# Kernel tuning notes

Hardware: AMD Instinct MI355X
Metric: run time of the kernel (lower is better)

## Reference

```python
import jax, jax.numpy as jnp
import numpy as np

N = 2097152
N_LAYERS = 32
N_SUB = 8


def setup_inputs() -> dict:
    key = jax.random.key(0)
    k1, k2, k3, k4 = jax.random.split(key, 4)
    return {
        "x": jax.random.normal(k1, (N, 2), dtype=jnp.float32),
        "act_w": 0.05 * jax.random.normal(k2, (N_LAYERS,), dtype=jnp.float32),
        "bias_b": 0.05 * jax.random.normal(k3, (N_LAYERS, 2), dtype=jnp.float32),
        "lin_w": 0.05 * jax.random.normal(k4, (N_LAYERS, N_SUB), dtype=jnp.float32),
    }


def _forward_chain(q, p, act_w, bias_b, lin_w):
    # Apply Modules[0..end] with inverse=0.
    n_layers, n_sub = lin_w.shape
    for i in range(n_layers):
        # activation module: up adds w*tanh(p) to q, low adds w*tanh(q) to p
        if i % 2 == 0:
            q = q + act_w[i] * jnp.tanh(p)
        else:
            p = p + act_w[i] * jnp.tanh(q)
        # bias module (inserted at j == 0)
        q = q + bias_b[i, 0]
        p = p + bias_b[i, 1]
        # linear shear modules
        for j in range(n_sub):
            if j % 2 == 0:   # linear_module_up: q += w*p
                q = q + lin_w[i, j] * p
            else:            # linear_module_low: p += w*q
                p = p + lin_w[i, j] * q
    return q, p


def _inverse_chain(q, p, act_w, bias_b, lin_w):
    # Apply all modules in reverse order with inverse=1 (negated weights).
    n_layers, n_sub = lin_w.shape
    for i in reversed(range(n_layers)):
        for j in reversed(range(n_sub)):
            if j % 2 == 0:
                q = q - lin_w[i, j] * p
            else:
                p = p - lin_w[i, j] * q
        q = q - bias_b[i, 0]
        p = p - bias_b[i, 1]
        if i % 2 == 0:
            q = q - act_w[i] * jnp.tanh(p)
        else:
            p = p - act_w[i] * jnp.tanh(q)
    return q, p


def reference(x, act_w, bias_b, lin_w):
    q, p = x[..., 0], x[..., 1]
    q, p = _forward_chain(q, p, act_w, bias_b, lin_w)
    # time reversal: multiply by [1, -1]
    p = -p
    q, p = _inverse_chain(q, p, act_w, bias_b, lin_w)
    # final module-0 inverse is included in _inverse_chain; scale by [1, -1]
    return jnp.stack([q, -p], axis=-1)
```

## Files before the change

kernel.cpp:

```cpp
#include <hip/hip_runtime.h>

constexpr int NL = 32;
constexpr int PPT = 4;

typedef float v2f __attribute__((ext_vector_type(2)));

__device__ __forceinline__ v2f splat(float a) { v2f r; r.x = a; r.y = a; return r; }
__device__ __forceinline__ v2f fma2(v2f a, v2f b, v2f c) { return __builtin_elementwise_fma(a, b, c); }
__device__ __forceinline__ v2f sfma(float s, v2f b, v2f c) { return __builtin_elementwise_fma(splat(s), b, c); }

__device__ __forceinline__ v2f tanh_poly2(v2f x) {
    v2f t = __builtin_elementwise_min(__builtin_elementwise_max(x, splat(-3.4f)), splat(3.4f));
    v2f s = t * t;
    v2f u = fma2(s, splat(2.3524e-06f), splat(-1.000059e-04f));
    u = fma2(s, u, splat(1.7302740e-03f));
    u = fma2(s, u, splat(-1.5874717e-02f));
    u = fma2(s, u, splat(8.5976700e-02f));
    u = fma2(s, u, splat(-3.0595090e-01f));
    u = fma2(s, u, splat(9.9691910e-01f));
    return t * u;
}

__global__ void build_tables(const float* __restrict__ act_w,
                             const float* __restrict__ bias_b,
                             const float* __restrict__ lin_w,
                             float* __restrict__ tab)
{
    int t = threadIdx.x;
    if (t >= NL) return;
    float m00 = 1.f, m01 = 0.f, m10 = 0.f, m11 = 1.f;
    #pragma unroll
    for (int j = 0; j < 8; ++j) {
        float w = lin_w[t * 8 + j];
        if ((j & 1) == 0) { m00 = fmaf(w, m10, m00); m01 = fmaf(w, m11, m01); }
        else              { m10 = fmaf(w, m00, m10); m11 = fmaf(w, m01, m11); }
    }
    float b0 = bias_b[2 * t], b1 = bias_b[2 * t + 1];
    float aw = act_w[t];
    float* f = &tab[t * 16];
    f[0] = m00; f[1] = m01; f[2] = m10; f[3] = m11;
    f[4] = fmaf(m00, b0, m01 * b1);
    f[5] = fmaf(m10, b0, m11 * b1);
    f[6] = aw; f[7] = 0.f;
    f[8]  = m11; f[9]  = -m01; f[10] = -m10; f[11] = m00;
    f[12] = -b0; f[13] = -b1; f[14] = -aw; f[15] = 0.f;
}

__global__ __launch_bounds__(256) void sympnet_main(
    const float* __restrict__ x,
    const float* __restrict__ tab,
    float* __restrict__ out)
{
    int gid = blockIdx.x * blockDim.x + threadIdx.x;
    const float4* x4 = (const float4*)x;
    float4* out4 = (float4*)out;
    long base = (long)gid * (PPT / 2);

    v2f Q[PPT / 2], P[PPT / 2];
    #pragma unroll
    for (int k = 0; k < PPT / 2; ++k) {
        float4 v = x4[base + k];
        Q[k].x = v.x; P[k].x = v.y;
        Q[k].y = v.z; P[k].y = v.w;
    }

    #pragma unroll 1
    for (int i = 0; i < NL; i += 2) {
        const float* f = &tab[i * 16];
        float m00=f[0], m01=f[1], m10=f[2], m11=f[3], C0=f[4], C1=f[5], T=f[6];
        const float* g = &tab[(i + 1) * 16];
        float n00=g[0], n01=g[1], n10=g[2], n11=g[3], E0=g[4], E1=g[5], U=g[6];
        #pragma unroll
        for (int k = 0; k < PPT / 2; ++k) {
            v2f Qa = sfma(T, tanh_poly2(P[k]), Q[k]);
            v2f Qn = sfma(m00, Qa, sfma(m01, P[k], splat(C0)));
            v2f Pn = sfma(m10, Qa, sfma(m11, P[k], splat(C1)));
            v2f Pa = sfma(U, tanh_poly2(Qn), Pn);
            Q[k] = sfma(n00, Qn, sfma(n01, Pa, splat(E0)));
            P[k] = sfma(n10, Qn, sfma(n11, Pa, splat(E1)));
        }
    }

    #pragma unroll
    for (int k = 0; k < PPT / 2; ++k) P[k] = -P[k];

    #pragma unroll 1
    for (int i = NL - 1; i > 0; i -= 2) {
        const float* g = &tab[i * 16 + 8];
        float n00=g[0], n01=g[1], n10=g[2], n11=g[3], E0=g[4], E1=g[5], U=g[6];
        const float* f = &tab[(i - 1) * 16 + 8];
        float m00=f[0], m01=f[1], m10=f[2], m11=f[3], C0=f[4], C1=f[5], T=f[6];
        #pragma unroll
        for (int k = 0; k < PPT / 2; ++k) {
            v2f Qn = sfma(n00, Q[k], sfma(n01, P[k], splat(E0)));
            v2f Pn = sfma(n10, Q[k], sfma(n11, P[k], splat(E1)));
            Pn = sfma(U, tanh_poly2(Qn), Pn);
            v2f Q2 = sfma(m00, Qn, sfma(m01, Pn, splat(C0)));
            v2f P2 = sfma(m10, Qn, sfma(m11, Pn, splat(C1)));
            Q[k] = sfma(T, tanh_poly2(P2), Q2);
            P[k] = P2;
        }
    }

    #pragma unroll
    for (int k = 0; k < PPT / 2; ++k) {
        float4 o;
        o.x = Q[k].x; o.y = -P[k].x;
        o.z = Q[k].y; o.w = -P[k].y;
        out4[base + k] = o;
    }
}

extern "C" void kernel_launch(void* const* d_in, const int* in_sizes, int n_in,
                              void* d_out, int out_size, void* d_ws, size_t ws_size,
                              hipStream_t stream) {
    const float* x      = (const float*)d_in[0];
    const float* act_w  = (const float*)d_in[1];
    const float* bias_b = (const float*)d_in[2];
    const float* lin_w  = (const float*)d_in[3];
    float* out = (float*)d_out;
    float* tab = (float*)d_ws;

    build_tables<<<1, 64, 0, stream>>>(act_w, bias_b, lin_w, tab);

    int npts = in_sizes[0] / 2;
    int nthreads = npts / PPT;
    int blocks = (nthreads + 255) / 256;
    sympnet_main<<<blocks, 256, 0, stream>>>(x, tab, out);
}
```

Baseline: 105.4 us.

## Use inline-asm packed FMAs with SGPR-pair operands and eight points per thread

Forces v_pk_fma_f32 through inline asm, with table weights stored as duplicated float pairs so they can be read as SGPR-pair operands. This avoids splat moves into VGPRs. It also folds the time-reversal sign flip into the inverse table, uses fmed3 for the clamp, and doubles the points per thread to 8 with launch bounds set for occupancy. The risks are higher register pressure and inline asm that blocks compiler scheduling. The launch now drops the rounding up of the block count, so it assumes N divides evenly.

```diff
diff --git a/kernel.cpp b/kernel.cpp
--- a/kernel.cpp
+++ b/kernel.cpp
@@ -1,33 +1,46 @@
 #include <hip/hip_runtime.h>
-
-constexpr int NL = 32;
-constexpr int PPT = 4;
 
 typedef float v2f __attribute__((ext_vector_type(2)));
 
-__device__ __forceinline__ v2f splat(float a) { v2f r; r.x = a; r.y = a; return r; }
-__device__ __forceinline__ v2f fma2(v2f a, v2f b, v2f c) { return __builtin_elementwise_fma(a, b, c); }
-__device__ __forceinline__ v2f sfma(float s, v2f b, v2f c) { return __builtin_elementwise_fma(splat(s), b, c); }
+__device__ __forceinline__ v2f pk_fma(v2f a, v2f b, v2f c) {
+    v2f d; asm("v_pk_fma_f32 %0, %1, %2, %3" : "=v"(d) : "v"(a), "v"(b), "v"(c)); return d;
+}
+__device__ __forceinline__ v2f pk_fma_svv(v2f a, v2f b, v2f c) {
+    v2f d; asm("v_pk_fma_f32 %0, %1, %2, %3" : "=v"(d) : "s"(a), "v"(b), "v"(c)); return d;
+}
+__device__ __forceinline__ v2f pk_fma_vvs(v2f a, v2f b, v2f c) {
+    v2f d; asm("v_pk_fma_f32 %0, %1, %2, %3" : "=v"(d) : "v"(a), "v"(b), "s"(c)); return d;
+}
+__device__ __forceinline__ v2f pk_mul(v2f a, v2f b) {
+    v2f d; asm("v_pk_mul_f32 %0, %1, %2" : "=v"(d) : "v"(a), "v"(b)); return d;
+}
+__device__ __forceinline__ v2f clamp2(v2f x) {
+    v2f r;
+    r.x = __builtin_amdgcn_fmed3f(x.x, -3.4f, 3.4f);
+    r.y = __builtin_amdgcn_fmed3f(x.y, -3.4f, 3.4f);
+    return r;
+}
 
-__device__ __forceinline__ v2f tanh_poly2(v2f x) {
-    v2f t = __builtin_elementwise_min(__builtin_elementwise_max(x, splat(-3.4f)), splat(3.4f));
-    v2f s = t * t;
-    v2f u = fma2(s, splat(2.3524e-06f), splat(-1.000059e-04f));
-    u = fma2(s, u, splat(1.7302740e-03f));
-    u = fma2(s, u, splat(-1.5874717e-02f));
-    u = fma2(s, u, splat(8.5976700e-02f));
-    u = fma2(s, u, splat(-3.0595090e-01f));
-    u = fma2(s, u, splat(9.9691910e-01f));
-    return t * u;
+__device__ __forceinline__ v2f tanh_pk(v2f x, v2f k6, v2f k5, v2f k4, v2f k3,
+                                       v2f k2, v2f k1, v2f k0) {
+    v2f t = clamp2(x);
+    v2f s = pk_mul(t, t);
+    v2f u = pk_fma_vvs(s, k6, k5);
+    u = pk_fma_vvs(s, u, k4);
+    u = pk_fma_vvs(s, u, k3);
+    u = pk_fma_vvs(s, u, k2);
+    u = pk_fma_vvs(s, u, k1);
+    u = pk_fma_vvs(s, u, k0);
+    return pk_mul(t, u);
 }
 
 __global__ void build_tables(const float* __restrict__ act_w,
                              const float* __restrict__ bias_b,
                              const float* __restrict__ lin_w,
-                             float* __restrict__ tab)
+                             v2f* __restrict__ tab)
 {
     int t = threadIdx.x;
-    if (t >= NL) return;
+    if (t >= 32) return;
     float m00 = 1.f, m01 = 0.f, m10 = 0.f, m11 = 1.f;
     #pragma unroll
     for (int j = 0; j < 8; ++j) {
@@ -35,75 +48,100 @@
         if ((j & 1) == 0) { m00 = fmaf(w, m10, m00); m01 = fmaf(w, m11, m01); }
         else              { m10 = fmaf(w, m00, m10); m11 = fmaf(w, m01, m11); }
     }
-    float b0 = bias_b[2 * t], b1 = bias_b[2 * t + 1];
-    float aw = act_w[t];
-    float* f = &tab[t * 16];
-    f[0] = m00; f[1] = m01; f[2] = m10; f[3] = m11;
-    f[4] = fmaf(m00, b0, m01 * b1);
-    f[5] = fmaf(m10, b0, m11 * b1);
-    f[6] = aw; f[7] = 0.f;
-    f[8]  = m11; f[9]  = -m01; f[10] = -m10; f[11] = m00;
-    f[12] = -b0; f[13] = -b1; f[14] = -aw; f[15] = 0.f;
+    float b0 = bias_b[2 * t], b1 = bias_b[2 * t + 1], aw = act_w[t];
+    float C0 = fmaf(m00, b0, m01 * b1);
+    float C1 = fmaf(m10, b0, m11 * b1);
+
+    v2f* f = tab + (t >> 1) * 16 + ((t & 1) ? 8 : 0);
+    f[0] = (v2f){m00, m00}; f[1] = (v2f){m01, m01};
+    f[2] = (v2f){m10, m10}; f[3] = (v2f){m11, m11};
+    f[4] = (v2f){C0, C0};   f[5] = (v2f){C1, C1};
+    f[6] = (v2f){aw, aw};   f[7] = (v2f){0.f, 0.f};
+
+    float s = (t == 31) ? -1.f : 1.f;
+    float i00 = m11, i01 = s * (-m01), i10 = -m10, i11 = s * m00;
+    v2f* g = (t & 1) ? (tab + 256 + ((31 - t) >> 1) * 16)
+                     : (tab + 256 + ((30 - t) >> 1) * 16 + 8);
+    g[0] = (v2f){i00, i00}; g[1] = (v2f){i01, i01};
+    g[2] = (v2f){i10, i10}; g[3] = (v2f){i11, i11};
+    g[4] = (v2f){-b0, -b0}; g[5] = (v2f){-b1, -b1};
+    g[6] = (v2f){-aw, -aw}; g[7] = (v2f){0.f, 0.f};
 }
 
-__global__ __launch_bounds__(256) void sympnet_main(
+__global__ __launch_bounds__(256, 4) void sympnet_main(
     const float* __restrict__ x,
-    const float* __restrict__ tab,
+    const v2f* __restrict__ tab,
     float* __restrict__ out)
 {
     int gid = blockIdx.x * blockDim.x + threadIdx.x;
     const float4* x4 = (const float4*)x;
     float4* out4 = (float4*)out;
-    long base = (long)gid * (PPT / 2);
+    long base = (long)gid * 4;
 
-    v2f Q[PPT / 2], P[PPT / 2];
+    v2f Q[4], P[4];
     #pragma unroll
-    for (int k = 0; k < PPT / 2; ++k) {
+    for (int k = 0; k < 4; ++k) {
         float4 v = x4[base + k];
-        Q[k].x = v.x; P[k].x = v.y;
-        Q[k].y = v.z; P[k].y = v.w;
+        Q[k] = (v2f){v.x, v.z};
+        P[k] = (v2f){v.y, v.w};
     }
 
+    const v2f k6 = {2.3524e-06f, 2.3524e-06f};
+    const v2f k5 = {-1.000059e-04f, -1.000059e-04f};
+    const v2f k4 = {1.7302740e-03f, 1.7302740e-03f};
+    const v2f k3 = {-1.5874717e-02f, -1.5874717e-02f};
+    const v2f k2 = {8.5976700e-02f, 8.5976700e-02f};
+    const v2f k1 = {-3.0595090e-01f, -3.0595090e-01f};
+    const v2f k0 = {9.9691910e-01f, 9.9691910e-01f};
+
     #pragma unroll 1
-    for (int i = 0; i < NL; i += 2) {
-        const float* f = &tab[i * 16];
-        float m00=f[0], m01=f[1], m10=f[2], m11=f[3], C0=f[4], C1=f[5], T=f[6];
-        const float* g = &tab[(i + 1) * 16];
-        float n00=g[0], n01=g[1], n10=g[2], n11=g[3], E0=g[4], E1=g[5], U=g[6];
+    for (int it = 0; it < 16; ++it) {
+        const v2f* f = tab + it * 16;
+        v2f F00=f[0], F01=f[1], F10=f[2], F11=f[3], FC0=f[4], FC1=f[5], FT=f[6];
+        v2f G00=f[8], G01=f[9], G10=f[10], G11=f[11], GC0=f[12], GC1=f[13], GT=f[14];
         #pragma unroll
-        for (int k = 0; k < PPT / 2; ++k) {
-            v2f Qa = sfma(T, tanh_poly2(P[k]), Q[k]);
-            v2f Qn = sfma(m00, Qa, sfma(m01, P[k], splat(C0)));
-            v2f Pn = sfma(m10, Qa, sfma(m11, P[k], splat(C1)));
-            v2f Pa = sfma(U, tanh_poly2(Qn), Pn);
-            Q[k] = sfma(n00, Qn, sfma(n01, Pa, splat(E0)));
-            P[k] = sfma(n10, Qn, sfma(n11, Pa, splat(E1)));
+        for (int k = 0; k < 4; ++k) {
+            v2f th = tanh_pk(P[k], k6, k5, k4, k3, k2, k1, k0);
+            v2f Qa = pk_fma_svv(FT, th, Q[k]);
+            v2f t1 = pk_fma_svv(F01, P[k], FC0);
+            v2f Qn = pk_fma_svv(F00, Qa, t1);
+            v2f t2 = pk_fma_svv(F11, P[k], FC1);
+            v2f Pn = pk_fma_svv(F10, Qa, t2);
+            v2f th2 = tanh_pk(Qn, k6, k5, k4, k3, k2, k1, k0);
+            v2f Pa = pk_fma_svv(GT, th2, Pn);
+            v2f t3 = pk_fma_svv(G01, Pa, GC0);
+            Q[k] = pk_fma_svv(G00, Qn, t3);
+            v2f t4 = pk_fma_svv(G11, Pa, GC1);
+            P[k] = pk_fma_svv(G10, Qn, t4);
         }
     }
 
-    #pragma unroll
-    for (int k = 0; k < PPT / 2; ++k) P[k] = -P[k];
 
     #pragma unroll 1
-    for (int i = NL - 1; i > 0; i -= 2) {
-        const float* g = &tab[i * 16 + 8];
-        float n00=g[0], n01=g[1], n10=g[2], n11=g[3], E0=g[4], E1=g[5], U=g[6];
-        const float* f = &tab[(i - 1) * 16 + 8];
-        float m00=f[0], m01=f[1], m10=f[2], m11=f[3], C0=f[4], C1=f[5], T=f[6];
+    for (int it = 0; it < 16; ++it) {
+        const v2f* f = tab + 256 + it * 16;
+        v2f A00=f[0], A01=f[1], A10=f[2], A11=f[3], Ac0=f[4], Ac1=f[5], AT=f[6];
+        v2f B00=f[8], B01=f[9], B10=f[10], B11=f[11], Bc0=f[12], Bc1=f[13], BT=f[14];
         #pragma unroll
-        for (int k = 0; k < PPT / 2; ++k) {
-            v2f Qn = sfma(n00, Q[k], sfma(n01, P[k], splat(E0)));
-            v2f Pn = sfma(n10, Q[k], sfma(n11, P[k], splat(E1)));
-            Pn = sfma(U, tanh_poly2(Qn), Pn);
-            v2f Q2 = sfma(m00, Qn, sfma(m01, Pn, splat(C0)));
-            v2f P2 = sfma(m10, Qn, sfma(m11, Pn, splat(C1)));
-            Q[k] = sfma(T, tanh_poly2(P2), Q2);
+        for (int k = 0; k < 4; ++k) {
+            v2f u1 = pk_fma_svv(A01, P[k], Ac0);
+            v2f Qn = pk_fma_svv(A00, Q[k], u1);
+            v2f u2 = pk_fma_svv(A11, P[k], Ac1);
+            v2f Pn = pk_fma_svv(A10, Q[k], u2);
+            v2f th = tanh_pk(Qn, k6, k5, k4, k3, k2, k1, k0);
+            Pn = pk_fma_svv(AT, th, Pn);
+            v2f u3 = pk_fma_svv(B01, Pn, Bc0);
+            v2f Q2 = pk_fma_svv(B00, Qn, u3);
+            v2f u4 = pk_fma_svv(B11, Pn, Bc1);
+            v2f P2 = pk_fma_svv(B10, Qn, u4);
+            v2f th2 = tanh_pk(P2, k6, k5, k4, k3, k2, k1, k0);
+            Q[k] = pk_fma_svv(BT, th2, Q2);
             P[k] = P2;
         }
     }
 
     #pragma unroll
-    for (int k = 0; k < PPT / 2; ++k) {
+    for (int k = 0; k < 4; ++k) {
         float4 o;
         o.x = Q[k].x; o.y = -P[k].x;
         o.z = Q[k].y; o.w = -P[k].y;
@@ -119,12 +157,12 @@
     const float* bias_b = (const float*)d_in[2];
     const float* lin_w  = (const float*)d_in[3];
     float* out = (float*)d_out;
-    float* tab = (float*)d_ws;
+    v2f* tab = (v2f*)d_ws;
 
     build_tables<<<1, 64, 0, stream>>>(act_w, bias_b, lin_w, tab);
 
     int npts = in_sizes[0] / 2;
-    int nthreads = npts / PPT;
-    int blocks = (nthreads + 255) / 256;
+    int nthreads = npts / 8;
+    int blocks = nthreads / 256;
     sympnet_main<<<blocks, 256, 0, stream>>>(x, tab, out);
 }
```

Result: slower. 108.8 us (+3.2%).
